# Performance work log

Measured on AMD Instinct MI355X. Metric: run time of the kernel, lower is better.

Reference implementation:

```python
import jax, jax.numpy as jnp
import numpy as np

N = 100000
E = 1600000
F_IN = 64
ACT = 8
NEG_SLOPE = 0.2


def _p(key, shape, scale=0.1):
    return jax.random.normal(key, shape, dtype=jnp.float32) * scale


def setup_inputs() -> dict:
    key = jax.random.key(0)
    ks = jax.random.split(key, 20)
    x = jax.random.normal(ks[0], (N, F_IN), dtype=jnp.float32)
    edge_index = jax.random.randint(ks[1], (2, E), 0, N, dtype=jnp.int64)
    edge_attr = jax.random.normal(ks[2], (E, 2), dtype=jnp.float32)
    # conv1: in=64, heads=4, out=16 -> 64
    H1, C1 = 4, 16
    Wl1 = _p(ks[3], (F_IN, H1 * C1)); bl1 = jnp.zeros((H1 * C1,), jnp.float32)
    Wr1 = _p(ks[4], (F_IN, H1 * C1)); br1 = jnp.zeros((H1 * C1,), jnp.float32)
    We1 = _p(ks[5], (2, H1 * C1))
    att1 = _p(ks[6], (H1, C1))
    b1 = jnp.zeros((H1 * C1,), jnp.float32)
    # conv2: in=64, heads=2, out=32 -> 64
    H2, C2 = 2, 32
    Wl2 = _p(ks[7], (H1 * C1, H2 * C2)); bl2 = jnp.zeros((H2 * C2,), jnp.float32)
    Wr2 = _p(ks[8], (H1 * C1, H2 * C2)); br2 = jnp.zeros((H2 * C2,), jnp.float32)
    We2 = _p(ks[9], (2, H2 * C2))
    att2 = _p(ks[10], (H2, C2))
    b2 = jnp.zeros((H2 * C2,), jnp.float32)
    Wm = _p(ks[11], (H2 * C2, ACT)); bm = jnp.zeros((ACT,), jnp.float32)
    return dict(x=x, edge_index=edge_index, edge_attr=edge_attr,
                Wl1=Wl1, bl1=bl1, Wr1=Wr1, br1=br1, We1=We1, att1=att1, b1=b1,
                Wl2=Wl2, bl2=bl2, Wr2=Wr2, br2=br2, We2=We2, att2=att2, b2=b2,
                Wm=Wm, bm=bm)


def gatv2_layer(x, src, dst, ea, Wl, bl, Wr, br, We, att, b, n_nodes, heads, ch):
    """PyG GATv2Conv with concat=True, add_self_loops=True (fill_value='mean')."""
    # self loops: edge attr = mean of incoming edge attrs per node (0 if none)
    deg = jax.ops.segment_sum(jnp.ones((src.shape[0],), ea.dtype), dst, n_nodes)
    loop_attr = jax.ops.segment_sum(ea, dst, n_nodes) / jnp.maximum(deg, 1.0)[:, None]
    loop = jnp.arange(n_nodes, dtype=src.dtype)
    s = jnp.concatenate([src, loop]); d = jnp.concatenate([dst, loop])
    ea_full = jnp.concatenate([ea, loop_attr], axis=0)
    xl = (x @ Wl + bl).reshape(n_nodes, heads, ch)   # source transform
    xr = (x @ Wr + br).reshape(n_nodes, heads, ch)   # target transform
    ee = (ea_full @ We).reshape(-1, heads, ch)
    e = jax.nn.leaky_relu(xl[s] + xr[d] + ee, NEG_SLOPE)  # [E', H, C]
    logits = jnp.einsum('ehc,hc->eh', e, att)             # [E', H]
    # segment softmax over destination (every node has a self loop -> non-empty)
    m = jax.ops.segment_max(logits, d, n_nodes)
    expl = jnp.exp(logits - m[d])
    denom = jax.ops.segment_sum(expl, d, n_nodes)
    alpha = expl / (denom[d] + 1e-16)
    out = jax.ops.segment_sum(xl[s] * alpha[:, :, None], d, n_nodes)
    return out.reshape(n_nodes, heads * ch) + b


def reference(x, edge_index, edge_attr, Wl1, bl1, Wr1, br1, We1, att1, b1,
              Wl2, bl2, Wr2, br2, We2, att2, b2, Wm, bm):
    src, dst = edge_index[0], edge_index[1]
    h = jax.nn.relu(gatv2_layer(x, src, dst, edge_attr, Wl1, bl1, Wr1, br1,
                                We1, att1, b1, N, 4, 16))
    h = jax.nn.relu(gatv2_layer(h, src, dst, edge_attr, Wl2, bl2, Wr2, br2,
                                We2, att2, b2, N, 2, 32))
    return jnp.tanh(h @ Wm + bm)
```

## Files before the change

### kernel.cpp

```cpp
#include <hip/hip_runtime.h>
#include <hip/hip_bf16.h>


constexpr int CAP = 64;

static __device__ __forceinline__ float bf2f(__hip_bfloat16 v) { return __bfloat162float(v); }
static __device__ __forceinline__ float bits2f(unsigned int u) { return __uint_as_float(u << 16); }
static __device__ __forceinline__ unsigned int f2bfbits(float f) {
  unsigned int u = __float_as_uint(f);
  return ((u + 0x7FFFu + ((u >> 16) & 1u)) >> 16) & 0xFFFFu;
}
static __device__ __forceinline__ float bcast(float v, int k) {
  return __int_as_float(__builtin_amdgcn_readlane(__float_as_int(v), k));
}

template <int CTRL>
static __device__ __forceinline__ float dpp_add(float v) {
  int m = __builtin_amdgcn_update_dpp(0, __float_as_int(v), CTRL, 0xf, 0xf, false);
  return v + __int_as_float(m);
}
static __device__ __forceinline__ float row16_sum(float p) {
  p = dpp_add<0x128>(p);
  p = dpp_add<0x124>(p);
  p = dpp_add<0x122>(p);
  p = dpp_add<0x121>(p);
  return p;
}
static __device__ __forceinline__ float quad_sum(float p) {
  p = dpp_add<0xB1>(p);
  p = dpp_add<0x4E>(p);
  return p;
}
static __device__ __forceinline__ float wave64_sum(float p) {
  p = row16_sum(p);
  p += __shfl_xor(p, 16);
  p += __shfl_xor(p, 32);
  return p;
}

static __device__ __forceinline__ float4 bf4_to_f4(uint2 g) {
  float4 r;
  r.x = __uint_as_float(g.x << 16);
  r.y = __uint_as_float(g.x & 0xffff0000u);
  r.z = __uint_as_float(g.y << 16);
  r.w = __uint_as_float(g.y & 0xffff0000u);
  return r;
}

template <typename T> static __device__ __forceinline__ float ldv(const T* p, size_t i);
template <> __device__ __forceinline__ float ldv<float>(const float* p, size_t i) { return p[i]; }
template <> __device__ __forceinline__ float ldv<__hip_bfloat16>(const __hip_bfloat16* p, size_t i) {
  return bf2f(p[i]);
}
template <typename T> static __device__ __forceinline__ void stv(T* p, size_t i, float v);
template <> __device__ __forceinline__ void stv<float>(float* p, size_t i, float v) { p[i] = v; }
template <> __device__ __forceinline__ void stv<__hip_bfloat16>(__hip_bfloat16* p, size_t i,
                                                                float v) {
  p[i] = __float2bfloat16(v);
}

__global__ void k_count(const int* __restrict__ dst, int* __restrict__ cnt, int E, int N) {
  int i = blockIdx.x * 256 + threadIdx.x;
  if (i >= E) return;
  int d = dst[i]; d = min(max(d, 0), N - 1);
  atomicAdd(&cnt[d], 1);
}

__global__ __launch_bounds__(1024) void k_scan_local(const int* __restrict__ deg,
                                                     int* __restrict__ off,
                                                     int* __restrict__ bsum, int n) {
  __shared__ int s[1024];
  int t = threadIdx.x;
  int g = blockIdx.x * 1024 + t;
  int v = (g < n) ? deg[g] : 0;
  s[t] = v;
  __syncthreads();
  for (int o = 1; o < 1024; o <<= 1) {
    int add = (t >= o) ? s[t - o] : 0;
    __syncthreads();
    s[t] += add;
    __syncthreads();
  }
  if (g < n) off[g] = s[t] - v;
  if (t == 1023) bsum[blockIdx.x] = s[t];
}

__global__ __launch_bounds__(256) void k_scan_part(const int* __restrict__ bsum,
                                                   int* __restrict__ boff,
                                                   int* __restrict__ off, int nb, int n) {
  __shared__ int s[256];
  int t = threadIdx.x;
  int v = (t < nb) ? bsum[t] : 0;
  s[t] = v;
  __syncthreads();
  for (int o = 1; o < 256; o <<= 1) {
    int add = (t >= o) ? s[t - o] : 0;
    __syncthreads();
    s[t] += add;
    __syncthreads();
  }
  if (t < nb) boff[t] = s[t] - v;
  if (t == nb - 1) off[n] = s[t];
}

__global__ __launch_bounds__(1024) void k_scan_add(int* __restrict__ off, int* __restrict__ cursor,
                                                   const int* __restrict__ boff, int n) {
  int g = blockIdx.x * 1024 + threadIdx.x;
  if (g < n) {
    int v = off[g] + boff[blockIdx.x];
    off[g] = v;
    cursor[g] = v;
  }
}

template <bool BUCKET>
__global__ void k_scatter(const int* __restrict__ src, const int* __restrict__ dst,
                          const float* __restrict__ ea, int* __restrict__ cursor,
                          long long* __restrict__ csr, int E, int N) {
  int i0 = (blockIdx.x * 256 + threadIdx.x) * 4;
  if (i0 >= E) return;
  if (i0 + 4 <= E) {
    int4 sv = *(const int4*)(src + i0);
    int4 dv = *(const int4*)(dst + i0);
    float4 ea01 = *(const float4*)(ea + 2 * i0);
    float4 ea23 = *(const float4*)(ea + 2 * i0 + 4);
    int ss[4] = {sv.x, sv.y, sv.z, sv.w};
    int dd[4] = {dv.x, dv.y, dv.z, dv.w};
    float e0[4] = {ea01.x, ea01.z, ea23.x, ea23.z};
    float e1[4] = {ea01.y, ea01.w, ea23.y, ea23.w};
    long long rec[4];
    int slot[4], d[4];
#pragma unroll
    for (int j = 0; j < 4; ++j) {
      d[j] = min(max(dd[j], 0), N - 1);
      int s = min(max(ss[j], 0), N - 1);
      unsigned int ep = f2bfbits(e0[j]) | (f2bfbits(e1[j]) << 16);
      rec[j] = (long long)(unsigned int)s | ((long long)ep << 32);
    }
#pragma unroll
    for (int j = 0; j < 4; ++j) slot[j] = atomicAdd(&cursor[d[j]], 1);
#pragma unroll
    for (int j = 0; j < 4; ++j) {
      if (BUCKET) {
        if (slot[j] < CAP) csr[(long long)d[j] * CAP + slot[j]] = rec[j];
      } else {
        csr[slot[j]] = rec[j];
      }
    }
  } else {
    for (int i = i0; i < E; ++i) {
      int d = min(max(dst[i], 0), N - 1);
      int s = min(max(src[i], 0), N - 1);
      unsigned int ep = f2bfbits(ea[2 * i]) | (f2bfbits(ea[2 * i + 1]) << 16);
      long long rec = (long long)(unsigned int)s | ((long long)ep << 32);
      int slot = atomicAdd(&cursor[d], 1);
      if (BUCKET) {
        if (slot < CAP) csr[(long long)d * CAP + slot] = rec;
      } else {
        csr[slot] = rec;
      }
    }
  }
}

__global__ __launch_bounds__(256) void k_gemm_xlxr(const float* __restrict__ in,
                                                   const float* __restrict__ Wl,
                                                   const float* __restrict__ bl,
                                                   const float* __restrict__ Wr,
                                                   const float* __restrict__ br,
                                                   unsigned short* __restrict__ xlb,
                                                   float* __restrict__ xr, int n) {
  int lane = threadIdx.x & 63, wave = threadIdx.x >> 6;
  float wl[64], wr[64];
#pragma unroll
  for (int k = 0; k < 64; ++k) {
    wl[k] = Wl[k * 64 + lane];
    wr[k] = Wr[k * 64 + lane];
  }
  float blc = bl[lane], brc = br[lane];
  const int stride = gridDim.x * 4;
  int node = blockIdx.x * 4 + wave;
  if (node >= n) return;
  float xv = in[(size_t)node * 64 + lane];
  while (node < n) {
    int nxt = node + stride;
    float xn = (nxt < n) ? in[(size_t)nxt * 64 + lane] : 0.f;
    float accl = blc, accr = brc;
#pragma unroll
    for (int k = 0; k < 64; ++k) {
      float s = bcast(xv, k);
      accl = fmaf(s, wl[k], accl);
      accr = fmaf(s, wr[k], accr);
    }
    xlb[(size_t)node * 64 + lane] = (unsigned short)f2bfbits(accl);
    xr[(size_t)node * 64 + lane] = accr;
    node = nxt;
    xv = xn;
  }
}

template <int C, bool FUSE_MLP, bool BUCKET>
__global__ __launch_bounds__(256) void k_agg4(const unsigned short* __restrict__ xlb,
                                              const float* __restrict__ xr,
                                              const long long* __restrict__ csr,
                                              const int* __restrict__ off,
                                              const int* __restrict__ cnt,
                                              const float* __restrict__ We,
                                              const float* __restrict__ att,
                                              const float* __restrict__ b,
                                              const float* __restrict__ Wm,
                                              const float* __restrict__ bm,
                                              float* __restrict__ hout,
                                              float* __restrict__ fout, int n) {
  int wid = (int)((blockIdx.x * blockDim.x + threadIdx.x) >> 6);
  int lane = threadIdx.x & 63;
  if (wid >= n) return;
  const int node = __builtin_amdgcn_readfirstlane(wid);
  const int sub = lane & 15;
  const int grp = lane >> 4;
  const int grp4 = grp << 2;

  float4 xr4 = ((const float4*)(xr + (size_t)node * 64))[sub];
  float4 We04 = ((const float4*)We)[sub];
  float4 We14 = ((const float4*)(We + 64))[sub];
  float4 att4 = ((const float4*)att)[sub];

  int dg, start, end;
  if (BUCKET) {
    dg = cnt[node];
    start = node * CAP;
    end = start + min(dg, CAP);
  } else {
    start = off[node];
    end = off[node + 1];
    dg = end - start;
  }

  float den = 0.f;
  float4 num = {0.f, 0.f, 0.f, 0.f};
  float ea0acc = 0.f, ea1acc = 0.f;

  for (int base = start; base < end; base += 64) {
    int c64 = min(64, end - base);
    long long meta = (lane < c64) ? __builtin_nontemporal_load(&csr[base + lane]) : 0LL;
    int mlo = (int)(unsigned long long)meta;
    int mhi = (int)((unsigned long long)meta >> 32);
    ea0acc += __uint_as_float((unsigned)mhi << 16);
    ea1acc += __uint_as_float((unsigned)mhi & 0xffff0000u);

    int iters = (c64 + 3) >> 2;
    int se0 = __builtin_amdgcn_ds_bpermute(grp4, mlo);
    int ep0 = __builtin_amdgcn_ds_bpermute(grp4, mhi);
    uint2 xg0 = ((const uint2*)(xlb + (size_t)(unsigned)se0 * 64))[sub];
    for (int t = 0; t < iters; ++t) {
      int ep1 = 0;
      uint2 xg1 = {0u, 0u};
      if (t + 1 < iters) {
        int idx = ((t + 1) << 4) + grp4;
        int se1 = __builtin_amdgcn_ds_bpermute(idx, mlo);
        ep1 = __builtin_amdgcn_ds_bpermute(idx, mhi);
        xg1 = ((const uint2*)(xlb + (size_t)(unsigned)se1 * 64))[sub];
      }
      float4 xc = bf4_to_f4(xg0);
      unsigned epc = (unsigned)ep0;
      float ea0 = __uint_as_float(epc << 16);
      float ea1 = __uint_as_float(epc & 0xffff0000u);
      float4 e;
      e.x = fmaf(ea1, We14.x, fmaf(ea0, We04.x, xc.x + xr4.x));
      e.y = fmaf(ea1, We14.y, fmaf(ea0, We04.y, xc.y + xr4.y));
      e.z = fmaf(ea1, We14.z, fmaf(ea0, We04.z, xc.z + xr4.z));
      e.w = fmaf(ea1, We14.w, fmaf(ea0, We04.w, xc.w + xr4.w));
      e.x = fmaxf(e.x, 0.2f * e.x);
      e.y = fmaxf(e.y, 0.2f * e.y);
      e.z = fmaxf(e.z, 0.2f * e.z);
      e.w = fmaxf(e.w, 0.2f * e.w);
      float p = e.x * att4.x;
      p = fmaf(e.y, att4.y, p);
      p = fmaf(e.z, att4.z, p);
      p = fmaf(e.w, att4.w, p);
      p = quad_sum(p);
      if (C == 32) p += __shfl_xor(p, 4);
      bool valid = ((t << 2) + grp) < c64;
      float ex = valid ? __expf(p) : 0.f;
      den += ex;
      num.x = fmaf(ex, xc.x, num.x);
      num.y = fmaf(ex, xc.y, num.y);
      num.z = fmaf(ex, xc.z, num.z);
      num.w = fmaf(ex, xc.w, num.w);
      ep0 = ep1;
      xg0 = xg1;
    }
  }

  den += __shfl_xor(den, 16);
  den += __shfl_xor(den, 32);
  num.x += __shfl_xor(num.x, 16); num.x += __shfl_xor(num.x, 32);
  num.y += __shfl_xor(num.y, 16); num.y += __shfl_xor(num.y, 32);
  num.z += __shfl_xor(num.z, 16); num.z += __shfl_xor(num.z, 32);
  num.w += __shfl_xor(num.w, 16); num.w += __shfl_xor(num.w, 32);

  float4 xls4 = bf4_to_f4(((const uint2*)(xlb + (size_t)node * 64))[sub]);
  {
    float s0 = wave64_sum(ea0acc);
    float s1 = wave64_sum(ea1acc);
    float inv = 1.0f / (float)max(dg, 1);
    float a0 = s0 * inv, a1 = s1 * inv;
    float4 e;
    e.x = fmaf(a1, We14.x, fmaf(a0, We04.x, xls4.x + xr4.x));
    e.y = fmaf(a1, We14.y, fmaf(a0, We04.y, xls4.y + xr4.y));
    e.z = fmaf(a1, We14.z, fmaf(a0, We04.z, xls4.z + xr4.z));
    e.w = fmaf(a1, We14.w, fmaf(a0, We04.w, xls4.w + xr4.w));
    e.x = fmaxf(e.x, 0.2f * e.x);
    e.y = fmaxf(e.y, 0.2f * e.y);
    e.z = fmaxf(e.z, 0.2f * e.z);
    e.w = fmaxf(e.w, 0.2f * e.w);
    float p = e.x * att4.x;
    p = fmaf(e.y, att4.y, p);
    p = fmaf(e.z, att4.z, p);
    p = fmaf(e.w, att4.w, p);
    p = quad_sum(p);
    if (C == 32) p += __shfl_xor(p, 4);
    float ex = __expf(p);
    den += ex;
    num.x = fmaf(ex, xls4.x, num.x);
    num.y = fmaf(ex, xls4.y, num.y);
    num.z = fmaf(ex, xls4.z, num.z);
    num.w = fmaf(ex, xls4.w, num.w);
  }

  float4 b4 = ((const float4*)b)[sub];
  float inv = 1.0f / (den + 1e-16f);
  float4 o;
  o.x = fmaxf(fmaf(num.x, inv, b4.x), 0.f);
  o.y = fmaxf(fmaf(num.y, inv, b4.y), 0.f);
  o.z = fmaxf(fmaf(num.z, inv, b4.z), 0.f);
  o.w = fmaxf(fmaf(num.w, inv, b4.w), 0.f);

  if (!FUSE_MLP) {
    if (grp == 0) ((float4*)(hout + (size_t)node * 64))[sub] = o;
  } else {
    float4 wr0a = *(const float4*)(Wm + (4 * sub + 0) * 8);
    float4 wr0b = *(const float4*)(Wm + (4 * sub + 0) * 8 + 4);
    float4 wr1a = *(const float4*)(Wm + (4 * sub + 1) * 8);
    float4 wr1b = *(const float4*)(Wm + (4 * sub + 1) * 8 + 4);
    float4 wr2a = *(const float4*)(Wm + (4 * sub + 2) * 8);
    float4 wr2b = *(const float4*)(Wm + (4 * sub + 2) * 8 + 4);
    float4 wr3a = *(const float4*)(Wm + (4 * sub + 3) * 8);
    float4 wr3b = *(const float4*)(Wm + (4 * sub + 3) * 8 + 4);
    const float* w0 = (const float*)&wr0a;
    const float* w0h = (const float*)&wr0b;
    const float* w1 = (const float*)&wr1a;
    const float* w1h = (const float*)&wr1b;
    const float* w2 = (const float*)&wr2a;
    const float* w2h = (const float*)&wr2b;
    const float* w3 = (const float*)&wr3a;
    const float* w3h = (const float*)&wr3b;
    float mine = 0.f;
#pragma unroll
    for (int j = 0; j < 8; ++j) {
      float c0 = (j < 4) ? w0[j & 3] : w0h[j & 3];
      float c1 = (j < 4) ? w1[j & 3] : w1h[j & 3];
      float c2 = (j < 4) ? w2[j & 3] : w2h[j & 3];
      float c3 = (j < 4) ? w3[j & 3] : w3h[j & 3];
      float p = o.x * c0;
      p = fmaf(o.y, c1, p);
      p = fmaf(o.z, c2, p);
      p = fmaf(o.w, c3, p);
      p = row16_sum(p);
      if (lane == j) mine = p;
    }
    if (lane < 8) fout[(size_t)node * 8 + lane] = tanhf(mine + bm[lane]);
  }
}

template <typename TIN, typename TOUT>
__global__ __launch_bounds__(256) void k_gemm_gen(const TIN* __restrict__ in,
                                                  const float* __restrict__ Wl,
                                                  const float* __restrict__ bl,
                                                  const float* __restrict__ Wr,
                                                  const float* __restrict__ br,
                                                  TOUT* __restrict__ xl, TOUT* __restrict__ xr,
                                                  int n) {
  int lane = threadIdx.x & 63, wave = threadIdx.x >> 6;
  float wl[64], wr[64];
#pragma unroll
  for (int k = 0; k < 64; ++k) {
    wl[k] = Wl[k * 64 + lane];
    wr[k] = Wr[k * 64 + lane];
  }
  float blc = bl[lane], brc = br[lane];
  for (int node = blockIdx.x * 4 + wave; node < n; node += gridDim.x * 4) {
    float xv = ldv(in, (size_t)node * 64 + lane);
    float accl = blc, accr = brc;
#pragma unroll
    for (int k = 0; k < 64; ++k) {
      float s = bcast(xv, k);
      accl = fmaf(s, wl[k], accl);
      accr = fmaf(s, wr[k], accr);
    }
    stv(xl, (size_t)node * 64 + lane, accl);
    stv(xr, (size_t)node * 64 + lane, accr);
  }
}

template <int C, bool FUSE_MLP, typename ST>
__global__ __launch_bounds__(256) void k_agg(const ST* __restrict__ xl, const ST* __restrict__ xr,
                                             const long long* __restrict__ csr,
                                             const int* __restrict__ off,
                                             const float* __restrict__ We,
                                             const float* __restrict__ att,
                                             const float* __restrict__ b,
                                             const float* __restrict__ Wm,
                                             const float* __restrict__ bm, ST* __restrict__ hout,
                                             float* __restrict__ fout, int n) {
  int wid = (int)((blockIdx.x * blockDim.x + threadIdx.x) >> 6);
  int lane = threadIdx.x & 63;
  if (wid >= n) return;
  const int node = __builtin_amdgcn_readfirstlane(wid);
  float xr_c = ldv(xr, (size_t)node * 64 + lane);
  float xl_self = ldv(xl, (size_t)node * 64 + lane);
  float We0 = We[lane], We1 = We[64 + lane], attc = att[lane], bc = b[lane];
  int start = off[node], end = off[node + 1], dg = end - start;
  float den = 0.f, num = 0.f, ea0acc = 0.f, ea1acc = 0.f;
  for (int base = start; base < end; base += 64) {
    int c64 = min(64, end - base);
    long long meta = (lane < c64) ? csr[base + lane] : 0;
    int mlo = (int)(unsigned long long)meta;
    int mhi = (int)((unsigned long long)meta >> 32);
    ea0acc += bits2f((unsigned)mhi & 0xffffu);
    ea1acc += bits2f((unsigned)mhi >> 16);
    for (int t = 0; t < c64; ++t) {
      int s = __builtin_amdgcn_readlane(mlo, t);
      unsigned ep = (unsigned)__builtin_amdgcn_readlane(mhi, t);
      float xls = ldv(xl, (size_t)s * 64 + lane);
      float e = xls + xr_c + bits2f(ep & 0xffffu) * We0 + bits2f(ep >> 16) * We1;
      e = fmaxf(e, 0.2f * e);
      float p = row16_sum(e * attc);
      if (C == 32) p += __shfl_xor(p, 16);
      float ex = __expf(p);
      den += ex;
      num = fmaf(ex, xls, num);
    }
  }
  {
    float s0 = wave64_sum(ea0acc), s1 = wave64_sum(ea1acc);
    float inv = 1.0f / (float)max(dg, 1);
    float e = xl_self + xr_c + s0 * inv * We0 + s1 * inv * We1;
    e = fmaxf(e, 0.2f * e);
    float p = row16_sum(e * attc);
    if (C == 32) p += __shfl_xor(p, 16);
    float ex = __expf(p);
    den += ex;
    num = fmaf(ex, xl_self, num);
  }
  float o = fmaxf(num / (den + 1e-16f) + bc, 0.f);
  if (!FUSE_MLP) {
    stv(hout, (size_t)node * 64 + lane, o);
  } else {
    float mine = 0.f;
#pragma unroll
    for (int j = 0; j < 8; ++j) {
      float p = wave64_sum(o * Wm[lane * 8 + j]);
      if (lane == j) mine = p;
    }
    if (lane < 8) fout[(size_t)node * 8 + lane] = tanhf(mine + bm[lane]);
  }
}

extern "C" void kernel_launch(void* const* d_in, const int* in_sizes, int n_in,
                              void* d_out, int out_size, void* d_ws, size_t ws_size,
                              hipStream_t stream) {
  const float* x = (const float*)d_in[0];
  const int* ei = (const int*)d_in[1];
  const float* ea = (const float*)d_in[2];
  const float* Wl1 = (const float*)d_in[3];
  const float* bl1 = (const float*)d_in[4];
  const float* Wr1 = (const float*)d_in[5];
  const float* br1 = (const float*)d_in[6];
  const float* We1 = (const float*)d_in[7];
  const float* att1 = (const float*)d_in[8];
  const float* b1 = (const float*)d_in[9];
  const float* Wl2 = (const float*)d_in[10];
  const float* bl2 = (const float*)d_in[11];
  const float* Wr2 = (const float*)d_in[12];
  const float* br2 = (const float*)d_in[13];
  const float* We2 = (const float*)d_in[14];
  const float* att2 = (const float*)d_in[15];
  const float* b2 = (const float*)d_in[16];
  const float* Wm = (const float*)d_in[17];
  const float* bm = (const float*)d_in[18];
  float* out = (float*)d_out;

  const int N = in_sizes[0] / 64;
  const int E = in_sizes[1] / 2;
  const int* src = ei;
  const int* dst = ei + E;

  auto al = [](size_t x) { return (x + 255) & ~(size_t)255; };
  const size_t needA = al((size_t)N * 4) + al((size_t)N * CAP * 8) + al((size_t)N * 64 * 2) +
                       al((size_t)N * 64 * 4) + al((size_t)N * 64 * 4);
  const size_t fixedB = al((size_t)N * 4) + al((size_t)(N + 1) * 4) + al((size_t)N * 4) +
                        al(1024) + al(1024) + al((size_t)E * 8);
  const size_t needB = fixedB + al((size_t)N * 64 * 2) + 2 * al((size_t)N * 64 * 4);

  char* p = (char*)d_ws;
  auto alloc = [&](size_t bytes) {
    char* r = p;
    p += (bytes + 255) & ~(size_t)255;
    return r;
  };

  const int egrid4 = (E + 1023) / 1024;
  const int egrid = (E + 255) / 256;
  const int agrid = (N + 3) / 4;
  const int ggrid = 1024;
  const int NB = (N + 1023) / 1024;

  if (ws_size >= needA) {
    int* cnt = (int*)alloc((size_t)N * 4);
    long long* csr = (long long*)alloc((size_t)N * CAP * 8);
    unsigned short* xlb = (unsigned short*)alloc((size_t)N * 64 * 2);
    float* xr = (float*)alloc((size_t)N * 64 * 4);
    float* h = (float*)alloc((size_t)N * 64 * 4);

    hipMemsetAsync(cnt, 0, (size_t)N * 4, stream);
    k_scatter<true><<<egrid4, 256, 0, stream>>>(src, dst, ea, cnt, csr, E, N);

    k_gemm_xlxr<<<ggrid, 256, 0, stream>>>(x, Wl1, bl1, Wr1, br1, xlb, xr, N);
    k_agg4<16, false, true><<<agrid, 256, 0, stream>>>(xlb, xr, csr, nullptr, cnt, We1, att1, b1,
                                                       nullptr, nullptr, h, nullptr, N);
    k_gemm_xlxr<<<ggrid, 256, 0, stream>>>(h, Wl2, bl2, Wr2, br2, xlb, xr, N);
    k_agg4<32, true, true><<<agrid, 256, 0, stream>>>(xlb, xr, csr, nullptr, cnt, We2, att2, b2,
                                                      Wm, bm, nullptr, out, N);
  } else if (ws_size >= needB) {
    int* cnt = (int*)alloc((size_t)N * 4);
    int* off = (int*)alloc((size_t)(N + 1) * 4);
    int* cursor = (int*)alloc((size_t)N * 4);
    int* bsum = (int*)alloc(1024);
    int* boff = (int*)alloc(1024);
    long long* csr = (long long*)alloc((size_t)E * 8);
    unsigned short* xlb = (unsigned short*)alloc((size_t)N * 64 * 2);
    float* xr = (float*)alloc((size_t)N * 64 * 4);
    float* h = (float*)alloc((size_t)N * 64 * 4);

    hipMemsetAsync(cnt, 0, (size_t)N * 4, stream);
    k_count<<<egrid, 256, 0, stream>>>(dst, cnt, E, N);
    k_scan_local<<<NB, 1024, 0, stream>>>(cnt, off, bsum, N);
    k_scan_part<<<1, 256, 0, stream>>>(bsum, boff, off, NB, N);
    k_scan_add<<<NB, 1024, 0, stream>>>(off, cursor, boff, N);
    k_scatter<false><<<egrid4, 256, 0, stream>>>(src, dst, ea, cursor, csr, E, N);

    k_gemm_xlxr<<<ggrid, 256, 0, stream>>>(x, Wl1, bl1, Wr1, br1, xlb, xr, N);
    k_agg4<16, false, false><<<agrid, 256, 0, stream>>>(xlb, xr, csr, off, nullptr, We1, att1, b1,
                                                        nullptr, nullptr, h, nullptr, N);
    k_gemm_xlxr<<<ggrid, 256, 0, stream>>>(h, Wl2, bl2, Wr2, br2, xlb, xr, N);
    k_agg4<32, true, false><<<agrid, 256, 0, stream>>>(xlb, xr, csr, off, nullptr, We2, att2, b2,
                                                       Wm, bm, nullptr, out, N);
  } else {
    int* cnt = (int*)alloc((size_t)N * 4);
    int* off = (int*)alloc((size_t)(N + 1) * 4);
    int* cursor = (int*)alloc((size_t)N * 4);
    int* bsum = (int*)alloc(1024);
    int* boff = (int*)alloc(1024);
    long long* csr = (long long*)alloc((size_t)E * 8);
    __hip_bfloat16* xl = (__hip_bfloat16*)alloc((size_t)N * 64 * 2);
    __hip_bfloat16* xr = (__hip_bfloat16*)alloc((size_t)N * 64 * 2);
    __hip_bfloat16* h = (__hip_bfloat16*)alloc((size_t)N * 64 * 2);

    hipMemsetAsync(cnt, 0, (size_t)N * 4, stream);
    k_count<<<egrid, 256, 0, stream>>>(dst, cnt, E, N);
    k_scan_local<<<NB, 1024, 0, stream>>>(cnt, off, bsum, N);
    k_scan_part<<<1, 256, 0, stream>>>(bsum, boff, off, NB, N);
    k_scan_add<<<NB, 1024, 0, stream>>>(off, cursor, boff, N);
    k_scatter<false><<<egrid4, 256, 0, stream>>>(src, dst, ea, cursor, csr, E, N);

    k_gemm_gen<float, __hip_bfloat16><<<ggrid, 256, 0, stream>>>(x, Wl1, bl1, Wr1, br1, xl, xr, N);
    k_agg<16, false, __hip_bfloat16><<<agrid, 256, 0, stream>>>(xl, xr, csr, off, We1, att1, b1,
                                                                nullptr, nullptr, h, nullptr, N);
    k_gemm_gen<__hip_bfloat16, __hip_bfloat16><<<ggrid, 256, 0, stream>>>(h, Wl2, bl2, Wr2, br2,
                                                                          xl, xr, N);
    k_agg<32, true, __hip_bfloat16><<<agrid, 256, 0, stream>>>(xl, xr, csr, off, We2, att2, b2,
                                                               Wm, bm, nullptr, out, N);
  }
}
```

Before: 517.2 us.

## Partition bucket scatter by destination range and make aggregation a persistent grid-stride loop

The bucketed scatter now launches 8x blocks. Each group handles only the edges whose destinations fall in one eighth of the node range, which localizes the atomics and CSR writes to a smaller memory region at the cost of reading the edge arrays eight times. The aggregation kernel becomes a persistent grid-stride loop over nodes with a fixed grid of 2048 blocks. This hoists the weight, attention and bias loads out of the per-node work and issues the self-node xl load early. The non-bucket paths use a simpler one-edge-per-thread scatter kernel.

```diff
diff --git a/kernel.cpp b/kernel.cpp
--- a/kernel.cpp
+++ b/kernel.cpp
@@ -113,11 +113,14 @@
   }
 }
 
-template <bool BUCKET>
-__global__ void k_scatter(const int* __restrict__ src, const int* __restrict__ dst,
-                          const float* __restrict__ ea, int* __restrict__ cursor,
-                          long long* __restrict__ csr, int E, int N) {
-  int i0 = (blockIdx.x * 256 + threadIdx.x) * 4;
+__global__ void k_scatter_x(const int* __restrict__ src, const int* __restrict__ dst,
+                            const float* __restrict__ ea, int* __restrict__ cursor,
+                            long long* __restrict__ csr, int E, int N) {
+  const int group = blockIdx.x & 7;
+  const int chunk = blockIdx.x >> 3;
+  const int r0 = (int)(((long long)N * group) >> 3);
+  const int r1 = (int)(((long long)N * (group + 1)) >> 3);
+  int i0 = (chunk * 256 + threadIdx.x) * 4;
   if (i0 >= E) return;
   if (i0 + 4 <= E) {
     int4 sv = *(const int4*)(src + i0);
@@ -128,39 +131,42 @@
     int dd[4] = {dv.x, dv.y, dv.z, dv.w};
     float e0[4] = {ea01.x, ea01.z, ea23.x, ea23.z};
     float e1[4] = {ea01.y, ea01.w, ea23.y, ea23.w};
-    long long rec[4];
-    int slot[4], d[4];
 #pragma unroll
     for (int j = 0; j < 4; ++j) {
-      d[j] = min(max(dd[j], 0), N - 1);
-      int s = min(max(ss[j], 0), N - 1);
-      unsigned int ep = f2bfbits(e0[j]) | (f2bfbits(e1[j]) << 16);
-      rec[j] = (long long)(unsigned int)s | ((long long)ep << 32);
-    }
-#pragma unroll
-    for (int j = 0; j < 4; ++j) slot[j] = atomicAdd(&cursor[d[j]], 1);
-#pragma unroll
-    for (int j = 0; j < 4; ++j) {
-      if (BUCKET) {
-        if (slot[j] < CAP) csr[(long long)d[j] * CAP + slot[j]] = rec[j];
-      } else {
-        csr[slot[j]] = rec[j];
+      int d = min(max(dd[j], 0), N - 1);
+      if (d >= r0 && d < r1) {
+        int s = min(max(ss[j], 0), N - 1);
+        unsigned int ep = f2bfbits(e0[j]) | (f2bfbits(e1[j]) << 16);
+        long long rec = (long long)(unsigned int)s | ((long long)ep << 32);
+        int slot = atomicAdd(&cursor[d], 1);
+        if (slot < CAP) csr[(long long)d * CAP + slot] = rec;
       }
     }
   } else {
     for (int i = i0; i < E; ++i) {
       int d = min(max(dst[i], 0), N - 1);
-      int s = min(max(src[i], 0), N - 1);
-      unsigned int ep = f2bfbits(ea[2 * i]) | (f2bfbits(ea[2 * i + 1]) << 16);
-      long long rec = (long long)(unsigned int)s | ((long long)ep << 32);
-      int slot = atomicAdd(&cursor[d], 1);
-      if (BUCKET) {
+      if (d >= r0 && d < r1) {
+        int s = min(max(src[i], 0), N - 1);
+        unsigned int ep = f2bfbits(ea[2 * i]) | (f2bfbits(ea[2 * i + 1]) << 16);
+        long long rec = (long long)(unsigned int)s | ((long long)ep << 32);
+        int slot = atomicAdd(&cursor[d], 1);
         if (slot < CAP) csr[(long long)d * CAP + slot] = rec;
-      } else {
-        csr[slot] = rec;
       }
     }
   }
+}
+
+__global__ void k_scatter_d(const int* __restrict__ src, const int* __restrict__ dst,
+                            const float* __restrict__ ea, int* __restrict__ cursor,
+                            long long* __restrict__ csr, int E, int N) {
+  int i = blockIdx.x * 256 + threadIdx.x;
+  if (i >= E) return;
+  int d = min(max(dst[i], 0), N - 1);
+  int s = min(max(src[i], 0), N - 1);
+  unsigned int ep = f2bfbits(ea[2 * i]) | (f2bfbits(ea[2 * i + 1]) << 16);
+  long long rec = (long long)(unsigned int)s | ((long long)ep << 32);
+  int slot = atomicAdd(&cursor[d], 1);
+  csr[slot] = rec;
 }
 
 __global__ __launch_bounds__(256) void k_gemm_xlxr(const float* __restrict__ in,
@@ -212,64 +218,107 @@
                                               const float* __restrict__ bm,
                                               float* __restrict__ hout,
                                               float* __restrict__ fout, int n) {
-  int wid = (int)((blockIdx.x * blockDim.x + threadIdx.x) >> 6);
-  int lane = threadIdx.x & 63;
-  if (wid >= n) return;
-  const int node = __builtin_amdgcn_readfirstlane(wid);
+  const int lane = threadIdx.x & 63;
   const int sub = lane & 15;
   const int grp = lane >> 4;
   const int grp4 = grp << 2;
 
-  float4 xr4 = ((const float4*)(xr + (size_t)node * 64))[sub];
-  float4 We04 = ((const float4*)We)[sub];
-  float4 We14 = ((const float4*)(We + 64))[sub];
-  float4 att4 = ((const float4*)att)[sub];
-
-  int dg, start, end;
-  if (BUCKET) {
-    dg = cnt[node];
-    start = node * CAP;
-    end = start + min(dg, CAP);
-  } else {
-    start = off[node];
-    end = off[node + 1];
-    dg = end - start;
-  }
-
-  float den = 0.f;
-  float4 num = {0.f, 0.f, 0.f, 0.f};
-  float ea0acc = 0.f, ea1acc = 0.f;
-
-  for (int base = start; base < end; base += 64) {
-    int c64 = min(64, end - base);
-    long long meta = (lane < c64) ? __builtin_nontemporal_load(&csr[base + lane]) : 0LL;
-    int mlo = (int)(unsigned long long)meta;
-    int mhi = (int)((unsigned long long)meta >> 32);
-    ea0acc += __uint_as_float((unsigned)mhi << 16);
-    ea1acc += __uint_as_float((unsigned)mhi & 0xffff0000u);
-
-    int iters = (c64 + 3) >> 2;
-    int se0 = __builtin_amdgcn_ds_bpermute(grp4, mlo);
-    int ep0 = __builtin_amdgcn_ds_bpermute(grp4, mhi);
-    uint2 xg0 = ((const uint2*)(xlb + (size_t)(unsigned)se0 * 64))[sub];
-    for (int t = 0; t < iters; ++t) {
-      int ep1 = 0;
-      uint2 xg1 = {0u, 0u};
-      if (t + 1 < iters) {
-        int idx = ((t + 1) << 4) + grp4;
-        int se1 = __builtin_amdgcn_ds_bpermute(idx, mlo);
-        ep1 = __builtin_amdgcn_ds_bpermute(idx, mhi);
-        xg1 = ((const uint2*)(xlb + (size_t)(unsigned)se1 * 64))[sub];
+  const float4 We04 = ((const float4*)We)[sub];
+  const float4 We14 = ((const float4*)(We + 64))[sub];
+  const float4 att4 = ((const float4*)att)[sub];
+  const float4 b4 = ((const float4*)b)[sub];
+
+  const int wstride = gridDim.x * 4;
+  for (int wid = blockIdx.x * 4 + (threadIdx.x >> 6); wid < n; wid += wstride) {
+    const int node = __builtin_amdgcn_readfirstlane(wid);
+    float4 xr4 = ((const float4*)(xr + (size_t)node * 64))[sub];
+    uint2 xself = ((const uint2*)(xlb + (size_t)node * 64))[sub];
+
+    int dg, start, end;
+    if (BUCKET) {
+      dg = cnt[node];
+      start = node * CAP;
+      end = start + min(dg, CAP);
+    } else {
+      start = off[node];
+      end = off[node + 1];
+      dg = end - start;
+    }
+
+    float den = 0.f;
+    float4 num = {0.f, 0.f, 0.f, 0.f};
+    float ea0acc = 0.f, ea1acc = 0.f;
+
+    for (int base = start; base < end; base += 64) {
+      int c64 = min(64, end - base);
+      long long meta = (lane < c64) ? __builtin_nontemporal_load(&csr[base + lane]) : 0LL;
+      int mlo = (int)(unsigned long long)meta;
+      int mhi = (int)((unsigned long long)meta >> 32);
+      ea0acc += __uint_as_float((unsigned)mhi << 16);
+      ea1acc += __uint_as_float((unsigned)mhi & 0xffff0000u);
+
+      int iters = (c64 + 3) >> 2;
+      int se0 = __builtin_amdgcn_ds_bpermute(grp4, mlo);
+      int ep0 = __builtin_amdgcn_ds_bpermute(grp4, mhi);
+      uint2 xg0 = ((const uint2*)(xlb + (size_t)(unsigned)se0 * 64))[sub];
+      for (int t = 0; t < iters; ++t) {
+        int ep1 = 0;
+        uint2 xg1 = {0u, 0u};
+        if (t + 1 < iters) {
+          int idx = ((t + 1) << 4) + grp4;
+          int se1 = __builtin_amdgcn_ds_bpermute(idx, mlo);
+          ep1 = __builtin_amdgcn_ds_bpermute(idx, mhi);
+          xg1 = ((const uint2*)(xlb + (size_t)(unsigned)se1 * 64))[sub];
+        }
+        float4 xc = bf4_to_f4(xg0);
+        unsigned epc = (unsigned)ep0;
+        float ea0 = __uint_as_float(epc << 16);
+        float ea1 = __uint_as_float(epc & 0xffff0000u);
+        float4 e;
+        e.x = fmaf(ea1, We14.x, fmaf(ea0, We04.x, xc.x + xr4.x));
+        e.y = fmaf(ea1, We14.y, fmaf(ea0, We04.y, xc.y + xr4.y));
+        e.z = fmaf(ea1, We14.z, fmaf(ea0, We04.z, xc.z + xr4.z));
+        e.w = fmaf(ea1, We14.w, fmaf(ea0, We04.w, xc.w + xr4.w));
+        e.x = fmaxf(e.x, 0.2f * e.x);
+        e.y = fmaxf(e.y, 0.2f * e.y);
+        e.z = fmaxf(e.z, 0.2f * e.z);
+        e.w = fmaxf(e.w, 0.2f * e.w);
+        float p = e.x * att4.x;
+        p = fmaf(e.y, att4.y, p);
+        p = fmaf(e.z, att4.z, p);
+        p = fmaf(e.w, att4.w, p);
+        p = quad_sum(p);
+        if (C == 32) p += __shfl_xor(p, 4);
+        bool valid = ((t << 2) + grp) < c64;
+        float ex = valid ? __expf(p) : 0.f;
+        den += ex;
+        num.x = fmaf(ex, xc.x, num.x);
+        num.y = fmaf(ex, xc.y, num.y);
+        num.z = fmaf(ex, xc.z, num.z);
+        num.w = fmaf(ex, xc.w, num.w);
+        ep0 = ep1;
+        xg0 = xg1;
       }
-      float4 xc = bf4_to_f4(xg0);
-      unsigned epc = (unsigned)ep0;
-      float ea0 = __uint_as_float(epc << 16);
-      float ea1 = __uint_as_float(epc & 0xffff0000u);
+    }
+
+    den += __shfl_xor(den, 16);
+    den += __shfl_xor(den, 32);
+    num.x += __shfl_xor(num.x, 16); num.x += __shfl_xor(num.x, 32);
+    num.y += __shfl_xor(num.y, 16); num.y += __shfl_xor(num.y, 32);
+    num.z += __shfl_xor(num.z, 16); num.z += __shfl_xor(num.z, 32);
+    num.w += __shfl_xor(num.w, 16); num.w += __shfl_xor(num.w, 32);
+
+    float4 xls4 = bf4_to_f4(xself);
+    {
+      float s0 = wave64_sum(ea0acc);
+      float s1 = wave64_sum(ea1acc);
+      float inv = 1.0f / (float)max(dg, 1);
+      float a0 = s0 * inv, a1 = s1 * inv;
       float4 e;
-      e.x = fmaf(ea1, We14.x, fmaf(ea0, We04.x, xc.x + xr4.x));
-      e.y = fmaf(ea1, We14.y, fmaf(ea0, We04.y, xc.y + xr4.y));
-      e.z = fmaf(ea1, We14.z, fmaf(ea0, We04.z, xc.z + xr4.z));
-      e.w = fmaf(ea1, We14.w, fmaf(ea0, We04.w, xc.w + xr4.w));
+      e.x = fmaf(a1, We14.x, fmaf(a0, We04.x, xls4.x + xr4.x));
+      e.y = fmaf(a1, We14.y, fmaf(a0, We04.y, xls4.y + xr4.y));
+      e.z = fmaf(a1, We14.z, fmaf(a0, We04.z, xls4.z + xr4.z));
+      e.w = fmaf(a1, We14.w, fmaf(a0, We04.w, xls4.w + xr4.w));
       e.x = fmaxf(e.x, 0.2f * e.x);
       e.y = fmaxf(e.y, 0.2f * e.y);
       e.z = fmaxf(e.z, 0.2f * e.z);
@@ -280,96 +329,56 @@
       p = fmaf(e.w, att4.w, p);
       p = quad_sum(p);
       if (C == 32) p += __shfl_xor(p, 4);
-      bool valid = ((t << 2) + grp) < c64;
-      float ex = valid ? __expf(p) : 0.f;
+      float ex = __expf(p);
       den += ex;
-      num.x = fmaf(ex, xc.x, num.x);
-      num.y = fmaf(ex, xc.y, num.y);
-      num.z = fmaf(ex, xc.z, num.z);
-      num.w = fmaf(ex, xc.w, num.w);
-      ep0 = ep1;
-      xg0 = xg1;
-    }
-  }
-
-  den += __shfl_xor(den, 16);
-  den += __shfl_xor(den, 32);
-  num.x += __shfl_xor(num.x, 16); num.x += __shfl_xor(num.x, 32);
-  num.y += __shfl_xor(num.y, 16); num.y += __shfl_xor(num.y, 32);
-  num.z += __shfl_xor(num.z, 16); num.z += __shfl_xor(num.z, 32);
-  num.w += __shfl_xor(num.w, 16); num.w += __shfl_xor(num.w, 32);
-
-  float4 xls4 = bf4_to_f4(((const uint2*)(xlb + (size_t)node * 64))[sub]);
-  {
-    float s0 = wave64_sum(ea0acc);
-    float s1 = wave64_sum(ea1acc);
-    float inv = 1.0f / (float)max(dg, 1);
-    float a0 = s0 * inv, a1 = s1 * inv;
-    float4 e;
-    e.x = fmaf(a1, We14.x, fmaf(a0, We04.x, xls4.x + xr4.x));
-    e.y = fmaf(a1, We14.y, fmaf(a0, We04.y, xls4.y + xr4.y));
-    e.z = fmaf(a1, We14.z, fmaf(a0, We04.z, xls4.z + xr4.z));
-    e.w = fmaf(a1, We14.w, fmaf(a0, We04.w, xls4.w + xr4.w));
-    e.x = fmaxf(e.x, 0.2f * e.x);
-    e.y = fmaxf(e.y, 0.2f * e.y);
-    e.z = fmaxf(e.z, 0.2f * e.z);
-    e.w = fmaxf(e.w, 0.2f * e.w);
-    float p = e.x * att4.x;
-    p = fmaf(e.y, att4.y, p);
-    p = fmaf(e.z, att4.z, p);
-    p = fmaf(e.w, att4.w, p);
-    p = quad_sum(p);
-    if (C == 32) p += __shfl_xor(p, 4);
-    float ex = __expf(p);
-    den += ex;
-    num.x = fmaf(ex, xls4.x, num.x);
-    num.y = fmaf(ex, xls4.y, num.y);
-    num.z = fmaf(ex, xls4.z, num.z);
-    num.w = fmaf(ex, xls4.w, num.w);
-  }
-
-  float4 b4 = ((const float4*)b)[sub];
-  float inv = 1.0f / (den + 1e-16f);
-  float4 o;
-  o.x = fmaxf(fmaf(num.x, inv, b4.x), 0.f);
-  o.y = fmaxf(fmaf(num.y, inv, b4.y), 0.f);
-  o.z = fmaxf(fmaf(num.z, inv, b4.z), 0.f);
-  o.w = fmaxf(fmaf(num.w, inv, b4.w), 0.f);
-
-  if (!FUSE_MLP) {
-    if (grp == 0) ((float4*)(hout + (size_t)node * 64))[sub] = o;
-  } else {
-    float4 wr0a = *(const float4*)(Wm + (4 * sub + 0) * 8);
-    float4 wr0b = *(const float4*)(Wm + (4 * sub + 0) * 8 + 4);
-    float4 wr1a = *(const float4*)(Wm + (4 * sub + 1) * 8);
-    float4 wr1b = *(const float4*)(Wm + (4 * sub + 1) * 8 + 4);
-    float4 wr2a = *(const float4*)(Wm + (4 * sub + 2) * 8);
-    float4 wr2b = *(const float4*)(Wm + (4 * sub + 2) * 8 + 4);
-    float4 wr3a = *(const float4*)(Wm + (4 * sub + 3) * 8);
-    float4 wr3b = *(const float4*)(Wm + (4 * sub + 3) * 8 + 4);
-    const float* w0 = (const float*)&wr0a;
-    const float* w0h = (const float*)&wr0b;
-    const float* w1 = (const float*)&wr1a;
-    const float* w1h = (const float*)&wr1b;
-    const float* w2 = (const float*)&wr2a;
-    const float* w2h = (const float*)&wr2b;
-    const float* w3 = (const float*)&wr3a;
-    const float* w3h = (const float*)&wr3b;
-    float mine = 0.f;
-#pragma unroll
-    for (int j = 0; j < 8; ++j) {
-      float c0 = (j < 4) ? w0[j & 3] : w0h[j & 3];
-      float c1 = (j < 4) ? w1[j & 3] : w1h[j & 3];
-      float c2 = (j < 4) ? w2[j & 3] : w2h[j & 3];
-      float c3 = (j < 4) ? w3[j & 3] : w3h[j & 3];
-      float p = o.x * c0;
-      p = fmaf(o.y, c1, p);
-      p = fmaf(o.z, c2, p);
-      p = fmaf(o.w, c3, p);
-      p = row16_sum(p);
-      if (lane == j) mine = p;
-    }
-    if (lane < 8) fout[(size_t)node * 8 + lane] = tanhf(mine + bm[lane]);
+      num.x = fmaf(ex, xls4.x, num.x);
+      num.y = fmaf(ex, xls4.y, num.y);
+      num.z = fmaf(ex, xls4.z, num.z);
+      num.w = fmaf(ex, xls4.w, num.w);
+    }
+
+    float inv = 1.0f / (den + 1e-16f);
+    float4 o;
+    o.x = fmaxf(fmaf(num.x, inv, b4.x), 0.f);
+    o.y = fmaxf(fmaf(num.y, inv, b4.y), 0.f);
+    o.z = fmaxf(fmaf(num.z, inv, b4.z), 0.f);
+    o.w = fmaxf(fmaf(num.w, inv, b4.w), 0.f);
+
+    if (!FUSE_MLP) {
+      if (grp == 0) ((float4*)(hout + (size_t)node * 64))[sub] = o;
+    } else {
+      float4 wr0a = *(const float4*)(Wm + (4 * sub + 0) * 8);
+      float4 wr0b = *(const float4*)(Wm + (4 * sub + 0) * 8 + 4);
+      float4 wr1a = *(const float4*)(Wm + (4 * sub + 1) * 8);
+      float4 wr1b = *(const float4*)(Wm + (4 * sub + 1) * 8 + 4);
+      float4 wr2a = *(const float4*)(Wm + (4 * sub + 2) * 8);
+      float4 wr2b = *(const float4*)(Wm + (4 * sub + 2) * 8 + 4);
+      float4 wr3a = *(const float4*)(Wm + (4 * sub + 3) * 8);
+      float4 wr3b = *(const float4*)(Wm + (4 * sub + 3) * 8 + 4);
+      const float* w0 = (const float*)&wr0a;
+      const float* w0h = (const float*)&wr0b;
+      const float* w1 = (const float*)&wr1a;
+      const float* w1h = (const float*)&wr1b;
+      const float* w2 = (const float*)&wr2a;
+      const float* w2h = (const float*)&wr2b;
+      const float* w3 = (const float*)&wr3a;
+      const float* w3h = (const float*)&wr3b;
+      float mine = 0.f;
+#pragma unroll
+      for (int j = 0; j < 8; ++j) {
+        float c0 = (j < 4) ? w0[j & 3] : w0h[j & 3];
+        float c1 = (j < 4) ? w1[j & 3] : w1h[j & 3];
+        float c2 = (j < 4) ? w2[j & 3] : w2h[j & 3];
+        float c3 = (j < 4) ? w3[j & 3] : w3h[j & 3];
+        float p = o.x * c0;
+        p = fmaf(o.y, c1, p);
+        p = fmaf(o.z, c2, p);
+        p = fmaf(o.w, c3, p);
+        p = row16_sum(p);
+        if (lane == j) mine = p;
+      }
+      if (lane < 8) fout[(size_t)node * 8 + lane] = tanhf(mine + bm[lane]);
+    }
   }
 }
 
@@ -512,7 +521,7 @@
 
   const int egrid4 = (E + 1023) / 1024;
   const int egrid = (E + 255) / 256;
-  const int agrid = (N + 3) / 4;
+  const int agrid = 2048;
   const int ggrid = 1024;
   const int NB = (N + 1023) / 1024;
 
@@ -524,7 +533,7 @@
     float* h = (float*)alloc((size_t)N * 64 * 4);
 
     hipMemsetAsync(cnt, 0, (size_t)N * 4, stream);
-    k_scatter<true><<<egrid4, 256, 0, stream>>>(src, dst, ea, cnt, csr, E, N);
+    k_scatter_x<<<egrid4 * 8, 256, 0, stream>>>(src, dst, ea, cnt, csr, E, N);
 
     k_gemm_xlxr<<<ggrid, 256, 0, stream>>>(x, Wl1, bl1, Wr1, br1, xlb, xr, N);
     k_agg4<16, false, true><<<agrid, 256, 0, stream>>>(xlb, xr, csr, nullptr, cnt, We1, att1, b1,
@@ -548,7 +557,7 @@
     k_scan_local<<<NB, 1024, 0, stream>>>(cnt, off, bsum, N);
     k_scan_part<<<1, 256, 0, stream>>>(bsum, boff, off, NB, N);
     k_scan_add<<<NB, 1024, 0, stream>>>(off, cursor, boff, N);
-    k_scatter<false><<<egrid4, 256, 0, stream>>>(src, dst, ea, cursor, csr, E, N);
+    k_scatter_d<<<egrid, 256, 0, stream>>>(src, dst, ea, cursor, csr, E, N);
 
     k_gemm_xlxr<<<ggrid, 256, 0, stream>>>(x, Wl1, bl1, Wr1, br1, xlb, xr, N);
     k_agg4<16, false, false><<<agrid, 256, 0, stream>>>(xlb, xr, csr, off, nullptr, We1, att1, b1,
@@ -572,14 +581,14 @@
     k_scan_local<<<NB, 1024, 0, stream>>>(cnt, off, bsum, N);
     k_scan_part<<<1, 256, 0, stream>>>(bsum, boff, off, NB, N);
     k_scan_add<<<NB, 1024, 0, stream>>>(off, cursor, boff, N);
-    k_scatter<false><<<egrid4, 256, 0, stream>>>(src, dst, ea, cursor, csr, E, N);
+    k_scatter_d<<<egrid, 256, 0, stream>>>(src, dst, ea, cursor, csr, E, N);
 
     k_gemm_gen<float, __hip_bfloat16><<<ggrid, 256, 0, stream>>>(x, Wl1, bl1, Wr1, br1, xl, xr, N);
-    k_agg<16, false, __hip_bfloat16><<<agrid, 256, 0, stream>>>(xl, xr, csr, off, We1, att1, b1,
-                                                                nullptr, nullptr, h, nullptr, N);
+    k_agg<16, false, __hip_bfloat16><<<(N + 3) / 4, 256, 0, stream>>>(
+        xl, xr, csr, off, We1, att1, b1, nullptr, nullptr, h, nullptr, N);
     k_gemm_gen<__hip_bfloat16, __hip_bfloat16><<<ggrid, 256, 0, stream>>>(h, Wl2, bl2, Wr2, br2,
                                                                           xl, xr, N);
-    k_agg<32, true, __hip_bfloat16><<<agrid, 256, 0, stream>>>(xl, xr, csr, off, We2, att2, b2,
-                                                               Wm, bm, nullptr, out, N);
-  }
-}
+    k_agg<32, true, __hip_bfloat16><<<(N + 3) / 4, 256, 0, stream>>>(
+        xl, xr, csr, off, We2, att2, b2, Wm, bm, nullptr, out, N);
+  }
+}
```

Measured after the change: 450.6 us. -12.9%, faster.
